# Performance work log

Hardware: AMD Instinct MI355X
Metric: run time of the kernel (lower is better)

The kernel has to match this reference:

```python
import jax, jax.numpy as jnp
import numpy as np

B, N_IN, D = 2, 262144, 32
N_OUT, K, NK = 65536, 4, 9
MIN_DIST = 0.01


def setup_inputs() -> dict:
    key = jax.random.key(0)
    k1, k2, k3, k4 = jax.random.split(key, 4)
    x_level_in = jax.random.normal(k1, (B, N_IN, D), dtype=jnp.float32)
    coords_in = jax.random.uniform(k2, (2, B, N_IN), dtype=jnp.float32)
    coords_out = jax.random.uniform(k3, (2, B, N_OUT, K), dtype=jnp.float32)
    neighbor_idx = jax.random.randint(k4, (B, N_OUT, K, NK), 0, N_IN)
    sigma = jnp.ones((D,), dtype=jnp.float32) * (MIN_DIST * 200.0)
    return {
        "x_level_in": x_level_in,
        "coords_in": coords_in,
        "coords_out": coords_out,
        "sigma": sigma,
        "neighbor_idx": neighbor_idx,
    }


def reference(x_level_in, coords_in, coords_out, sigma, neighbor_idx):
    # x_level_in: [B, N_in, D]; coords_in: [2, B, N_in]
    # coords_out: [2, B, N_out, K]; neighbor_idx: [B, N_out, K, NK]; sigma: [D]
    b = jnp.arange(x_level_in.shape[0])[:, None, None, None]  # batch index broadcaster
    # gather neighbor coordinates across the input grid: [2, B, N_out, K, NK]
    nb_coords = coords_in[:, b, neighbor_idx]
    # squared euclidean distance in (lon, lat): [B, N_out, K, NK]
    d2 = jnp.sum((coords_out[..., None] - nb_coords) ** 2, axis=0)
    # per-channel Gaussian/RBF weights: [B, N_out, K, NK, D]
    w = jnp.exp(-d2[..., None] / (2.0 * sigma ** 2))
    # gather neighbor features: [B, N_out, K, NK, D]
    feats = x_level_in[b, neighbor_idx]
    # normalized weighted aggregate over the NK neighbors: [B, N_out, K, D]
    num = jnp.sum(w * feats, axis=3)
    den = jnp.sum(w, axis=3) + 1e-9
    x = num / den
    # flatten (N_out, K) -> sequence dim, as in forward's final view
    return x.reshape(x.shape[0], -1, x.shape[-1])
```

## Files before the change

kernel.cpp:

```cpp
#include <hip/hip_runtime.h>
#include <hip/hip_fp16.h>

constexpr int B        = 2;
constexpr int N_IN     = 262144;
constexpr int D        = 32;
constexpr int N_OUT    = 65536;
constexpr int K        = 4;
constexpr int NK       = 9;
constexpr int P        = B * N_OUT * K;
constexpr int PPB      = N_OUT * K;
constexpr size_t XTOT  = (size_t)B * N_IN * D;

typedef _Float16 half2v __attribute__((ext_vector_type(2)));
typedef _Float16 half8v __attribute__((ext_vector_type(8)));
typedef float    f4v    __attribute__((ext_vector_type(4)));

template<int L>
__device__ __forceinline__ int qbcast_i(int v) {
    return __builtin_amdgcn_mov_dpp(v, L * 0x55, 0xf, 0xf, true);
}
template<int L>
__device__ __forceinline__ float qbcast_f(float v) {
    return __int_as_float(
        __builtin_amdgcn_mov_dpp(__float_as_int(v), L * 0x55, 0xf, 0xf, true));
}

__global__ __launch_bounds__(256) void cvt_fp16_kernel(
    const float* __restrict__ x, _Float16* __restrict__ xh)
{
    const size_t i = (size_t)(blockIdx.x * 256 + threadIdx.x) * 8;
    const float4 a = *reinterpret_cast<const float4*>(x + i);
    const float4 b = *reinterpret_cast<const float4*>(x + i + 4);
    half8v h;
    h[0] = (_Float16)a.x; h[1] = (_Float16)a.y;
    h[2] = (_Float16)a.z; h[3] = (_Float16)a.w;
    h[4] = (_Float16)b.x; h[5] = (_Float16)b.y;
    h[6] = (_Float16)b.z; h[7] = (_Float16)b.w;
    *reinterpret_cast<half8v*>(xh + i) = h;
}

__global__ __launch_bounds__(256) void pack_coords_kernel(
    const float* __restrict__ cin, half2v* __restrict__ cp)
{
    const int i = blockIdx.x * 256 + threadIdx.x;
    half2v h;
    h[0] = (_Float16)cin[i];
    h[1] = (_Float16)cin[B * N_IN + i];
    cp[i] = h;
}

__global__ __launch_bounds__(256) void projection_kernel_h(
    const _Float16* __restrict__ xh,
    const half2v*   __restrict__ cpack,
    const float*    __restrict__ coords_out,
    const float*    __restrict__ sigma,
    const int*      __restrict__ nidx,
    float*          __restrict__ out)
{
    const int bid   = blockIdx.x;
    const int xcd   = bid & 7;
    const int j     = bid >> 3;
    const int batch = xcd >> 2;
    const int bbi   = j * 4 + (xcd & 3);
    const int point = batch * PPB + bbi * 64 + (threadIdx.x >> 2);
    const int h     = threadIdx.x & 3;

    const int cbase = batch * N_IN;

    const float cox = __builtin_nontemporal_load(coords_out + point);
    const float coy = __builtin_nontemporal_load(coords_out + P + point);

    const float4 sg0 = *reinterpret_cast<const float4*>(sigma + h * 8);
    const float4 sg1 = *reinterpret_cast<const float4*>(sigma + h * 8 + 4);
    float s[8];
    s[0] = 1.0f / (2.0f * sg0.x * sg0.x); s[1] = 1.0f / (2.0f * sg0.y * sg0.y);
    s[2] = 1.0f / (2.0f * sg0.z * sg0.z); s[3] = 1.0f / (2.0f * sg0.w * sg0.w);
    s[4] = 1.0f / (2.0f * sg1.x * sg1.x); s[5] = 1.0f / (2.0f * sg1.y * sg1.y);
    s[6] = 1.0f / (2.0f * sg1.z * sg1.z); s[7] = 1.0f / (2.0f * sg1.w * sg1.w);
    bool uni = true;
    #pragma unroll
    for (int k = 1; k < 8; ++k) uni = uni && (s[k] == s[0]);

    const int* __restrict__ ip = nidx + (size_t)point * NK;
    const int ia = __builtin_nontemporal_load(ip + h);
    const int ib = __builtin_nontemporal_load(ip + 4 + h);
    const int i8 = __builtin_nontemporal_load(ip + 8);

    const half2v ca = cpack[cbase + ia];
    const half2v cb = cpack[cbase + ib];
    const half2v c8 = cpack[cbase + i8];

    int idxs[NK];
    idxs[0] = qbcast_i<0>(ia); idxs[1] = qbcast_i<1>(ia);
    idxs[2] = qbcast_i<2>(ia); idxs[3] = qbcast_i<3>(ia);
    idxs[4] = qbcast_i<0>(ib); idxs[5] = qbcast_i<1>(ib);
    idxs[6] = qbcast_i<2>(ib); idxs[7] = qbcast_i<3>(ib);
    idxs[8] = i8;

    half8v f[NK];
    #pragma unroll
    for (int t = 0; t < NK; ++t)
        f[t] = *reinterpret_cast<const half8v*>(
            xh + (size_t)(cbase + idxs[t]) * D + h * 8);

    const float dxa = cox - (float)ca[0], dya = coy - (float)ca[1];
    const float dxb = cox - (float)cb[0], dyb = coy - (float)cb[1];
    const float dx8 = cox - (float)c8[0], dy8 = coy - (float)c8[1];
    const float d2a = dxa * dxa + dya * dya;
    const float d2b = dxb * dxb + dyb * dyb;
    const float d28 = dx8 * dx8 + dy8 * dy8;

    float num[8];
    #pragma unroll
    for (int k = 0; k < 8; ++k) num[k] = 0.f;
    float den[8];
    #pragma unroll
    for (int k = 0; k < 8; ++k) den[k] = 0.f;

    if (uni) {
        const float wa = __expf(-d2a * s[0]);
        const float wb = __expf(-d2b * s[0]);
        const float w8 = __expf(-d28 * s[0]);
        float w[NK];
        w[0] = qbcast_f<0>(wa); w[1] = qbcast_f<1>(wa);
        w[2] = qbcast_f<2>(wa); w[3] = qbcast_f<3>(wa);
        w[4] = qbcast_f<0>(wb); w[5] = qbcast_f<1>(wb);
        w[6] = qbcast_f<2>(wb); w[7] = qbcast_f<3>(wb);
        w[8] = w8;
        float d0 = 0.f;
        #pragma unroll
        for (int t = 0; t < NK; ++t) {
            d0 += w[t];
            #pragma unroll
            for (int k = 0; k < 8; ++k) num[k] += w[t] * (float)f[t][k];
        }
        #pragma unroll
        for (int k = 0; k < 8; ++k) den[k] = d0;
    } else {
        float d2v[NK];
        d2v[0] = qbcast_f<0>(d2a); d2v[1] = qbcast_f<1>(d2a);
        d2v[2] = qbcast_f<2>(d2a); d2v[3] = qbcast_f<3>(d2a);
        d2v[4] = qbcast_f<0>(d2b); d2v[5] = qbcast_f<1>(d2b);
        d2v[6] = qbcast_f<2>(d2b); d2v[7] = qbcast_f<3>(d2b);
        d2v[8] = d28;
        #pragma unroll
        for (int t = 0; t < NK; ++t) {
            #pragma unroll
            for (int k = 0; k < 8; ++k) {
                const float w = __expf(-d2v[t] * s[k]);
                num[k] += w * (float)f[t][k];
                den[k] += w;
            }
        }
    }

    float* op = out + (size_t)point * D + h * 8;
    f4v o0, o1;
    o0.x = num[0] / (den[0] + 1e-9f); o0.y = num[1] / (den[1] + 1e-9f);
    o0.z = num[2] / (den[2] + 1e-9f); o0.w = num[3] / (den[3] + 1e-9f);
    o1.x = num[4] / (den[4] + 1e-9f); o1.y = num[5] / (den[5] + 1e-9f);
    o1.z = num[6] / (den[6] + 1e-9f); o1.w = num[7] / (den[7] + 1e-9f);
    __builtin_nontemporal_store(o0, reinterpret_cast<f4v*>(op));
    __builtin_nontemporal_store(o1, reinterpret_cast<f4v*>(op + 4));
}

__global__ __launch_bounds__(256) void projection_kernel_f32(
    const float* __restrict__ x,
    const float* __restrict__ coords_in,
    const float* __restrict__ coords_out,
    const float* __restrict__ sigma,
    const int*   __restrict__ nidx,
    float*       __restrict__ out)
{
    const int tid   = blockIdx.x * 256 + threadIdx.x;
    const int point = tid >> 3;
    const int q     = tid & 7;
    const int b     = point / PPB;
    const int cbase = b * N_IN;

    const float cox = coords_out[point];
    const float coy = coords_out[P + point];

    const float4 sg = *reinterpret_cast<const float4*>(sigma + q * 4);
    const float s0 = 1.0f / (2.0f * sg.x * sg.x);
    const float s1 = 1.0f / (2.0f * sg.y * sg.y);
    const float s2 = 1.0f / (2.0f * sg.z * sg.z);
    const float s3 = 1.0f / (2.0f * sg.w * sg.w);

    float4 num = make_float4(0.f, 0.f, 0.f, 0.f);
    float4 den = make_float4(0.f, 0.f, 0.f, 0.f);
    const int* __restrict__ ip = nidx + (size_t)point * NK;

    #pragma unroll
    for (int nk = 0; nk < NK; ++nk) {
        const int idx = ip[nk];
        const float cx = coords_in[cbase + idx];
        const float cy = coords_in[B * N_IN + cbase + idx];
        const float dx = cox - cx;
        const float dy = coy - cy;
        const float d2 = dx * dx + dy * dy;
        const float4 f = *reinterpret_cast<const float4*>(
            x + (size_t)(cbase + idx) * D + q * 4);
        const float w0 = __expf(-d2 * s0);
        const float w1 = __expf(-d2 * s1);
        const float w2 = __expf(-d2 * s2);
        const float w3 = __expf(-d2 * s3);
        num.x += w0 * f.x;  den.x += w0;
        num.y += w1 * f.y;  den.y += w1;
        num.z += w2 * f.z;  den.z += w2;
        num.w += w3 * f.w;  den.w += w3;
    }

    float4 o;
    o.x = num.x / (den.x + 1e-9f);
    o.y = num.y / (den.y + 1e-9f);
    o.z = num.z / (den.z + 1e-9f);
    o.w = num.w / (den.w + 1e-9f);
    *reinterpret_cast<float4*>(out + (size_t)point * D + q * 4) = o;
}

extern "C" void kernel_launch(void* const* d_in, const int* in_sizes, int n_in,
                              void* d_out, int out_size, void* d_ws, size_t ws_size,
                              hipStream_t stream) {
    const float* x      = (const float*)d_in[0];
    const float* cin    = (const float*)d_in[1];
    const float* cout_  = (const float*)d_in[2];
    const float* sigma  = (const float*)d_in[3];
    const int*   nidx   = (const int*)  d_in[4];
    float*       outp   = (float*)d_out;

    const int block = 256;

    const size_t xh_bytes = XTOT * sizeof(_Float16);
    const size_t cp_bytes = (size_t)B * N_IN * sizeof(half2v);

    if (ws_size >= xh_bytes + cp_bytes) {
        _Float16* xh = (_Float16*)d_ws;
        half2v*   cp = (half2v*)((char*)d_ws + xh_bytes);
        cvt_fp16_kernel<<<(int)(XTOT / 8 / block), block, 0, stream>>>(x, xh);
        pack_coords_kernel<<<(B * N_IN) / block, block, 0, stream>>>(cin, cp);
        const int grid_main = (P * 4) / block;
        projection_kernel_h<<<grid_main, block, 0, stream>>>(
            xh, cp, cout_, sigma, nidx, outp);
    } else {
        const int grid_main = (P * 8) / block;
        projection_kernel_f32<<<grid_main, block, 0, stream>>>(
            x, cin, cout_, sigma, nidx, outp);
    }
}
```

Measured before the change: 216.9 us.

## Phase neighbor feature gathers by index range and fuse prep kernels

In the uniform-sigma path, feature gathers are split into four phases by the high bits of the neighbor index, with block-wide barriers between phases. Each block then touches only one 65536-row slice of the fp16 feature table at a time, which is meant to improve L2 locality. The fp16 conversion and coordinate packing kernels are merged into one launch, and the division is replaced by a reciprocal multiply. In exchange, the gathers lose their upfront memory-level parallelism and the kernel pays for three __syncthreads per block.

```diff
diff --git a/kernel.cpp b/kernel.cpp
--- a/kernel.cpp
+++ b/kernel.cpp
@@ -10,6 +10,7 @@
 constexpr int P        = B * N_OUT * K;
 constexpr int PPB      = N_OUT * K;
 constexpr size_t XTOT  = (size_t)B * N_IN * D;
+constexpr int NPH      = 4;
 
 typedef _Float16 half2v __attribute__((ext_vector_type(2)));
 typedef _Float16 half8v __attribute__((ext_vector_type(8)));
@@ -25,28 +26,26 @@
         __builtin_amdgcn_mov_dpp(__float_as_int(v), L * 0x55, 0xf, 0xf, true));
 }
 
-__global__ __launch_bounds__(256) void cvt_fp16_kernel(
-    const float* __restrict__ x, _Float16* __restrict__ xh)
+__global__ __launch_bounds__(256) void prep_kernel(
+    const float* __restrict__ x,   _Float16* __restrict__ xh,
+    const float* __restrict__ cin, half2v*   __restrict__ cp)
 {
-    const size_t i = (size_t)(blockIdx.x * 256 + threadIdx.x) * 8;
-    const float4 a = *reinterpret_cast<const float4*>(x + i);
-    const float4 b = *reinterpret_cast<const float4*>(x + i + 4);
+    const int tid  = blockIdx.x * 256 + threadIdx.x;
+    const size_t i = (size_t)tid * 8;
+    const f4v a = __builtin_nontemporal_load(reinterpret_cast<const f4v*>(x + i));
+    const f4v b = __builtin_nontemporal_load(reinterpret_cast<const f4v*>(x + i) + 1);
     half8v h;
-    h[0] = (_Float16)a.x; h[1] = (_Float16)a.y;
-    h[2] = (_Float16)a.z; h[3] = (_Float16)a.w;
-    h[4] = (_Float16)b.x; h[5] = (_Float16)b.y;
-    h[6] = (_Float16)b.z; h[7] = (_Float16)b.w;
+    h[0] = (_Float16)a[0]; h[1] = (_Float16)a[1];
+    h[2] = (_Float16)a[2]; h[3] = (_Float16)a[3];
+    h[4] = (_Float16)b[0]; h[5] = (_Float16)b[1];
+    h[6] = (_Float16)b[2]; h[7] = (_Float16)b[3];
     *reinterpret_cast<half8v*>(xh + i) = h;
-}
-
-__global__ __launch_bounds__(256) void pack_coords_kernel(
-    const float* __restrict__ cin, half2v* __restrict__ cp)
-{
-    const int i = blockIdx.x * 256 + threadIdx.x;
-    half2v h;
-    h[0] = (_Float16)cin[i];
-    h[1] = (_Float16)cin[B * N_IN + i];
-    cp[i] = h;
+    if (tid < B * N_IN) {
+        half2v c;
+        c[0] = (_Float16)cin[tid];
+        c[1] = (_Float16)cin[B * N_IN + tid];
+        cp[tid] = c;
+    }
 }
 
 __global__ __launch_bounds__(256) void projection_kernel_h(
@@ -97,12 +96,6 @@
     idxs[6] = qbcast_i<2>(ib); idxs[7] = qbcast_i<3>(ib);
     idxs[8] = i8;
 
-    half8v f[NK];
-    #pragma unroll
-    for (int t = 0; t < NK; ++t)
-        f[t] = *reinterpret_cast<const half8v*>(
-            xh + (size_t)(cbase + idxs[t]) * D + h * 8);
-
     const float dxa = cox - (float)ca[0], dya = coy - (float)ca[1];
     const float dxb = cox - (float)cb[0], dyb = coy - (float)cb[1];
     const float dx8 = cox - (float)c8[0], dy8 = coy - (float)c8[1];
@@ -113,9 +106,6 @@
     float num[8];
     #pragma unroll
     for (int k = 0; k < 8; ++k) num[k] = 0.f;
-    float den[8];
-    #pragma unroll
-    for (int k = 0; k < 8; ++k) den[k] = 0.f;
 
     if (uni) {
         const float wa = __expf(-d2a * s[0]);
@@ -127,16 +117,36 @@
         w[4] = qbcast_f<0>(wb); w[5] = qbcast_f<1>(wb);
         w[6] = qbcast_f<2>(wb); w[7] = qbcast_f<3>(wb);
         w[8] = w8;
-        float d0 = 0.f;
+        float den = 0.f;
         #pragma unroll
-        for (int t = 0; t < NK; ++t) {
-            d0 += w[t];
+        for (int t = 0; t < NK; ++t) den += w[t];
+
+        for (int ph = 0; ph < NPH; ++ph) {
             #pragma unroll
-            for (int k = 0; k < 8; ++k) num[k] += w[t] * (float)f[t][k];
+            for (int t = 0; t < NK; ++t) {
+                if ((idxs[t] >> 16) == ph) {
+                    const half8v f = *reinterpret_cast<const half8v*>(
+                        xh + (size_t)(cbase + idxs[t]) * D + h * 8);
+                    #pragma unroll
+                    for (int k = 0; k < 8; ++k) num[k] += w[t] * (float)f[k];
+                }
+            }
+            if (ph != NPH - 1) __syncthreads();
         }
+
+        float* op = out + (size_t)point * D + h * 8;
+        const float r = 1.0f / (den + 1e-9f);
+        f4v o0, o1;
+        o0[0] = num[0] * r; o0[1] = num[1] * r;
+        o0[2] = num[2] * r; o0[3] = num[3] * r;
+        o1[0] = num[4] * r; o1[1] = num[5] * r;
+        o1[2] = num[6] * r; o1[3] = num[7] * r;
+        __builtin_nontemporal_store(o0, reinterpret_cast<f4v*>(op));
+        __builtin_nontemporal_store(o1, reinterpret_cast<f4v*>(op + 4));
+    } else {
+        float den[8];
         #pragma unroll
-        for (int k = 0; k < 8; ++k) den[k] = d0;
-    } else {
+        for (int k = 0; k < 8; ++k) den[k] = 0.f;
         float d2v[NK];
         d2v[0] = qbcast_f<0>(d2a); d2v[1] = qbcast_f<1>(d2a);
         d2v[2] = qbcast_f<2>(d2a); d2v[3] = qbcast_f<3>(d2a);
@@ -145,23 +155,24 @@
         d2v[8] = d28;
         #pragma unroll
         for (int t = 0; t < NK; ++t) {
+            const half8v f = *reinterpret_cast<const half8v*>(
+                xh + (size_t)(cbase + idxs[t]) * D + h * 8);
             #pragma unroll
             for (int k = 0; k < 8; ++k) {
-                const float w = __expf(-d2v[t] * s[k]);
-                num[k] += w * (float)f[t][k];
-                den[k] += w;
+                const float wk = __expf(-d2v[t] * s[k]);
+                num[k] += wk * (float)f[k];
+                den[k] += wk;
             }
         }
-    }
-
-    float* op = out + (size_t)point * D + h * 8;
-    f4v o0, o1;
-    o0.x = num[0] / (den[0] + 1e-9f); o0.y = num[1] / (den[1] + 1e-9f);
-    o0.z = num[2] / (den[2] + 1e-9f); o0.w = num[3] / (den[3] + 1e-9f);
-    o1.x = num[4] / (den[4] + 1e-9f); o1.y = num[5] / (den[5] + 1e-9f);
-    o1.z = num[6] / (den[6] + 1e-9f); o1.w = num[7] / (den[7] + 1e-9f);
-    __builtin_nontemporal_store(o0, reinterpret_cast<f4v*>(op));
-    __builtin_nontemporal_store(o1, reinterpret_cast<f4v*>(op + 4));
+        float* op = out + (size_t)point * D + h * 8;
+        f4v o0, o1;
+        o0[0] = num[0] / (den[0] + 1e-9f); o0[1] = num[1] / (den[1] + 1e-9f);
+        o0[2] = num[2] / (den[2] + 1e-9f); o0[3] = num[3] / (den[3] + 1e-9f);
+        o1[0] = num[4] / (den[4] + 1e-9f); o1[1] = num[5] / (den[5] + 1e-9f);
+        o1[2] = num[6] / (den[6] + 1e-9f); o1[3] = num[7] / (den[7] + 1e-9f);
+        __builtin_nontemporal_store(o0, reinterpret_cast<f4v*>(op));
+        __builtin_nontemporal_store(o1, reinterpret_cast<f4v*>(op + 4));
+    }
 }
 
 __global__ __launch_bounds__(256) void projection_kernel_f32(
@@ -237,8 +248,7 @@
     if (ws_size >= xh_bytes + cp_bytes) {
         _Float16* xh = (_Float16*)d_ws;
         half2v*   cp = (half2v*)((char*)d_ws + xh_bytes);
-        cvt_fp16_kernel<<<(int)(XTOT / 8 / block), block, 0, stream>>>(x, xh);
-        pack_coords_kernel<<<(B * N_IN) / block, block, 0, stream>>>(cin, cp);
+        prep_kernel<<<(int)(XTOT / 8 / block), block, 0, stream>>>(x, xh, cin, cp);
         const int grid_main = (P * 4) / block;
         projection_kernel_h<<<grid_main, block, 0, stream>>>(
             xh, cp, cout_, sigma, nidx, outp);
```

New measurement: 259.7 us. 19.7% more time.
